# Kernel optimization log

Measured on AMD Instinct MI355X. Metric: run time of the kernel, lower is better.

Reference implementation:

```python
import jax, jax.numpy as jnp
import numpy as np

ALPHA_MIN = 1e-6
SN_EPS = 1e-6


def _spectral_normalize(W, u):
    # One power iteration (torch spectral_norm, n_power_iterations=1).
    v = W.T @ u
    v = v / (jnp.linalg.norm(v) + SN_EPS)
    u1 = W @ v
    u1 = u1 / (jnp.linalg.norm(u1) + SN_EPS)
    u1 = jax.lax.stop_gradient(u1)
    v = jax.lax.stop_gradient(v)
    sigma = u1 @ (W @ v)
    return W / sigma


def setup_inputs() -> dict:
    key = jax.random.key(0)
    ks = jax.random.split(key, 11)
    B, T, D, K = 32, 2048, 512, 128
    x = jax.random.normal(ks[0], (B, T, D), jnp.float32)
    dt = jax.random.uniform(ks[1], (B, T), jnp.float32)
    alpha_mod = jax.random.normal(ks[2], (B, T, K), jnp.float32)
    omega_mod = jax.random.normal(ks[3], (B, T, K), jnp.float32)
    tau_mod = jax.random.normal(ks[4], (B, T, 1), jnp.float32)
    s_real_raw = jax.random.normal(ks[5], (K,), jnp.float32)
    s_imag = jax.random.normal(ks[6], (K,), jnp.float32)
    tau_raw = jax.random.normal(ks[7], (1,), jnp.float32)
    W_orig = jax.random.normal(ks[8], (K, D), jnp.float32) * (1.0 / np.sqrt(D))
    b = jax.random.normal(ks[9], (K,), jnp.float32) * 0.01
    u_sn = jax.random.normal(ks[10], (K,), jnp.float32)
    u_sn = u_sn / jnp.linalg.norm(u_sn)
    return {"x": x, "dt": dt, "alpha_mod": alpha_mod, "omega_mod": omega_mod,
            "tau_mod": tau_mod, "s_real_raw": s_real_raw, "s_imag": s_imag,
            "tau_raw": tau_raw, "W_orig": W_orig, "b": b, "u_sn": u_sn}


def reference(x, dt, alpha_mod, omega_mod, tau_mod, s_real_raw, s_imag,
              tau_raw, W_orig, b, u_sn):
    B, T, D = x.shape
    K = W_orig.shape[0]

    # global timescale and poles
    tau = jax.nn.softplus(tau_raw[0]) + 1e-3
    alpha0 = (jax.nn.softplus(s_real_raw) + ALPHA_MIN) * tau  # [K]
    omega0 = s_imag * tau                                      # [K]

    # time-varying modulation (all log-scale)
    scale = jnp.exp(tau_mod)                                   # [B,T,1]
    alpha = alpha0 * jnp.exp(alpha_mod) * scale                # [B,T,K]
    omega = omega0 * jnp.exp(omega_mod) * scale                # [B,T,K]

    dt3 = dt[..., None]                                        # [B,T,1]
    rho = jnp.exp(-alpha * dt3)                                # [B,T,K]
    theta = omega * dt3
    cos_t = jnp.cos(theta)
    sin_t = jnp.sin(theta)

    # spectral-norm projection u = x @ W_sn^T + b -> [B,T,K]
    W_sn = _spectral_normalize(W_orig, u_sn)
    u = jnp.einsum('btd,kd->btk', x, W_sn) + b

    # complex recurrence: z_t = rho_t * e^{i theta_t} * z_{t-1} + u_t
    def step(carry, inp):
        c, s = carry
        rt, ct, st, ut = inp
        c_new = rt * (c * ct - s * st) + ut
        s_new = rt * (c * st + s * ct)
        return (c_new, s_new), (c_new, s_new)

    xs = (jnp.swapaxes(rho, 0, 1), jnp.swapaxes(cos_t, 0, 1),
          jnp.swapaxes(sin_t, 0, 1), jnp.swapaxes(u, 0, 1))  # [T,B,K]
    init = (jnp.zeros((B, K), u.dtype), jnp.zeros((B, K), u.dtype))
    _, (C, S) = jax.lax.scan(step, init, xs)
    C = jnp.swapaxes(C, 0, 1)  # [B,T,K]
    S = jnp.swapaxes(S, 0, 1)
    return jnp.concatenate([C, S], axis=-1)  # [B,T,2K]
```

## Files before the change

### kernel.cpp

```cpp
#include <hip/hip_runtime.h>
#include <hip/hip_bf16.h>
#include <math.h>

typedef __bf16 bf16x8 __attribute__((ext_vector_type(8)));
typedef __bf16 bf16x4 __attribute__((ext_vector_type(4)));
typedef __bf16 bf16x2 __attribute__((ext_vector_type(2)));
typedef float f32x4 __attribute__((ext_vector_type(4)));

#define B_SZ 32
#define T_SZ 2048
#define D_SZ 512
#define K_SZ 128
#define TC 32
#define NC 64

__device__ __forceinline__ float softplus_f(float x){
  return x > 20.f ? x : log1pf(expf(x));
}

__global__ __launch_bounds__(512) void sn_pi(const float* __restrict__ W,
                                             const float* __restrict__ u_sn,
                                             float* __restrict__ sig_inv){
  __shared__ float red[512];
  __shared__ float vsh[512];
  __shared__ float ush[128];
  const int t = threadIdx.x;
  if (t < 128) ush[t] = u_sn[t];
  __syncthreads();
  float t1 = 0.f;
  #pragma unroll 8
  for (int k = 0; k < K_SZ; ++k) t1 += W[k*D_SZ + t] * ush[k];
  red[t] = t1 * t1;
  __syncthreads();
  for (int s = 256; s > 0; s >>= 1){ if (t < s) red[t] += red[t+s]; __syncthreads(); }
  const float n1 = sqrtf(red[0]);
  vsh[t] = t1 / (n1 + 1e-6f);
  __syncthreads();
  float t2 = 0.f;
  if (t < 128){
    const float4* Wr = (const float4*)(W + (size_t)t * D_SZ);
    const float4* vp = (const float4*)vsh;
    #pragma unroll 8
    for (int d = 0; d < D_SZ/4; ++d){
      const float4 a = Wr[d], v = vp[d];
      t2 += a.x*v.x + a.y*v.y + a.z*v.z + a.w*v.w;
    }
  }
  __syncthreads();
  red[t] = (t < 128) ? t2*t2 : 0.f;
  __syncthreads();
  for (int s = 256; s > 0; s >>= 1){ if (t < s) red[t] += red[t+s]; __syncthreads(); }
  if (t == 0){
    const float n2sq = red[0];
    const float sigma = n2sq / (sqrtf(n2sq) + 1e-6f);
    sig_inv[0] = 1.f / sigma;
  }
}

__global__ __launch_bounds__(256) void sn_scale(const float* __restrict__ W,
                                                const float* __restrict__ sig_inv,
                                                __bf16* __restrict__ Wb){
  const float inv = sig_inv[0];
  const int i = blockIdx.x*256 + threadIdx.x;
  const float4 v = ((const float4*)W)[i];
  bf16x4 o; o[0]=(__bf16)(v.x*inv); o[1]=(__bf16)(v.y*inv);
  o[2]=(__bf16)(v.z*inv); o[3]=(__bf16)(v.w*inv);
  ((bf16x4*)Wb)[i] = o;
}

__global__ __launch_bounds__(256) void gemm_xw(const float* __restrict__ X,
                                               const __bf16* __restrict__ Wb,
                                               __bf16* __restrict__ U){
  __shared__ bf16x8 As[2][1024];
  __shared__ bf16x8 Bs[2][1024];
  const int tid = threadIdx.x;
  const int lane = tid & 63;
  const int wid = tid >> 6;
  const int wm = wid >> 1, wn = wid & 1;
  const int rowbase = blockIdx.x * 128;
  const int L15 = lane & 15, Lq = lane >> 4;
  f32x4 acc[4][4] = {};

  const int rowA = tid >> 3;
  const int cg   = tid & 7;
  const int colo = cg * 8;
  int pidx[4];
  #pragma unroll
  for (int r = 0; r < 4; ++r){
    const int row = rowA + 32*r;
    const int fb = ((row >> 4) << 1) | (cg >> 2);
    const int ll = (row & 15) | ((cg & 3) << 4);
    pidx[r] = (fb*64 + ll) ^ cg;
  }
  const float* Xb  = X  + (size_t)(rowbase + rowA)*D_SZ + colo;
  const __bf16* Bb = Wb + (size_t)rowA*D_SZ + colo;

  float4 va[4], vb[4];
  bf16x8 wreg[4];
  #pragma unroll
  for (int r = 0; r < 4; ++r){
    const float4* q = (const float4*)(Xb + (size_t)(32*r)*D_SZ);
    va[r] = q[0]; vb[r] = q[1];
    wreg[r] = *(const bf16x8*)(Bb + (size_t)(32*r)*D_SZ);
  }

  int pb = 0;
  for (int kk = 0; kk < D_SZ; kk += 64){
    #pragma unroll
    for (int r = 0; r < 4; ++r){
      bf16x8 f;
      f[0]=(__bf16)va[r].x; f[1]=(__bf16)va[r].y; f[2]=(__bf16)va[r].z; f[3]=(__bf16)va[r].w;
      f[4]=(__bf16)vb[r].x; f[5]=(__bf16)vb[r].y; f[6]=(__bf16)vb[r].z; f[7]=(__bf16)vb[r].w;
      As[pb][pidx[r]] = f;
      Bs[pb][pidx[r]] = wreg[r];
    }
    __syncthreads();
    if (kk + 64 < D_SZ){
      #pragma unroll
      for (int r = 0; r < 4; ++r){
        const float4* q = (const float4*)(Xb + (size_t)(32*r)*D_SZ + kk + 64);
        va[r] = q[0]; vb[r] = q[1];
        wreg[r] = *(const bf16x8*)(Bb + (size_t)(32*r)*D_SZ + kk + 64);
      }
    }
    #pragma unroll
    for (int s = 0; s < 2; ++s){
      bf16x8 af[4], bfr[4];
      const int swz = (s << 2) | (lane >> 4);
      #pragma unroll
      for (int ii = 0; ii < 4; ++ii){
        const int fb = ((wm*4+ii) << 1) | s;
        af[ii] = As[pb][(fb*64 + lane) ^ swz];
      }
      #pragma unroll
      for (int jj = 0; jj < 4; ++jj){
        const int fb = ((wn*4+jj) << 1) | s;
        bfr[jj] = Bs[pb][(fb*64 + lane) ^ swz];
      }
      #pragma unroll
      for (int ii = 0; ii < 4; ++ii)
        #pragma unroll
        for (int jj = 0; jj < 4; ++jj)
          acc[ii][jj] = __builtin_amdgcn_mfma_f32_16x16x32_bf16(af[ii], bfr[jj], acc[ii][jj], 0, 0, 0);
    }
    pb ^= 1;
  }
  #pragma unroll
  for (int ii = 0; ii < 4; ++ii){
    const int m = rowbase + (wm*4+ii)*16 + (Lq << 2);
    #pragma unroll
    for (int jj = 0; jj < 4; ++jj){
      const int n = (wn*4+jj)*16 + L15;
      #pragma unroll
      for (int r = 0; r < 4; ++r)
        U[(size_t)(m + r)*K_SZ + n] = (__bf16)acc[ii][jj][r];
    }
  }
}

__global__ __launch_bounds__(256) void pass_a(
    const float* __restrict__ alpha_mod, const float* __restrict__ omega_mod,
    const __bf16* __restrict__ Uarr, const float* __restrict__ dt,
    const float* __restrict__ tau_mod, const float* __restrict__ s_real,
    const float* __restrict__ s_imag, const float* __restrict__ tau_raw,
    const float* __restrict__ bvec,
    float2* __restrict__ sumA, float2* __restrict__ sumT,
    float2* __restrict__ Zr, float2* __restrict__ Zi){
  const int t = threadIdx.x;
  const int kh = t & 63;
  const int cl = t >> 6;
  const int b = blockIdx.y;
  const int c = blockIdx.x*4 + cl;
  const int t0 = c * TC;
  __shared__ float sdt[4*TC], ssc[4*TC];
  if (t < 4*TC){
    const int tg = blockIdx.x*4*TC + t;
    sdt[t] = dt[b*T_SZ + tg];
    ssc[t] = __expf(tau_mod[b*T_SZ + tg]);
  }
  __syncthreads();
  const float tau = softplus_f(tau_raw[0]) + 1e-3f;
  const float2 sr = ((const float2*)s_real)[kh];
  const float2 si = ((const float2*)s_imag)[kh];
  const float2 bk = ((const float2*)bvec)[kh];
  const float a0[2] = {(softplus_f(sr.x)+1e-6f)*tau, (softplus_f(sr.y)+1e-6f)*tau};
  const float w0[2] = {si.x*tau, si.y*tau};
  float zr[2]={0,0}, zs[2]={0,0}, sA[2]={0,0}, sT[2]={0,0};
  const float* sd = sdt + cl*TC;
  const float* ss = ssc + cl*TC;
  const size_t row = (size_t)(b*T_SZ + t0);
  const float2* amp = (const float2*)(alpha_mod + row*K_SZ) + kh;
  const float2* omp = (const float2*)(omega_mod + row*K_SZ) + kh;
  const bf16x2* up  = (const bf16x2*)(Uarr + row*K_SZ) + kh;
  #pragma unroll 4
  for (int i = 0; i < TC; ++i){
    const float2 am = amp[(size_t)i*64];
    const float2 om = omp[(size_t)i*64];
    const bf16x2 u2 = up[(size_t)i*64];
    const float scdt = ss[i] * sd[i];
    #pragma unroll
    for (int j = 0; j < 2; ++j){
      const float ad = a0[j] * __expf(j ? am.y : am.x) * scdt;
      const float th = w0[j] * __expf(j ? om.y : om.x) * scdt;
      const float rho = __expf(-ad);
      float st, ct; __sincosf(th, &st, &ct);
      const float uu = (float)u2[j] + (j ? bk.y : bk.x);
      const float nr = rho*(zr[j]*ct - zs[j]*st) + uu;
      const float ns = rho*(zr[j]*st + zs[j]*ct);
      zr[j] = nr; zs[j] = ns;
      sA[j] += ad; sT[j] += th;
    }
  }
  const size_t idx = ((size_t)(b*NC + c))*64 + kh;
  sumA[idx] = make_float2(sA[0], sA[1]);
  sumT[idx] = make_float2(sT[0], sT[1]);
  Zr[idx]   = make_float2(zr[0], zr[1]);
  Zi[idx]   = make_float2(zs[0], zs[1]);
}

__global__ __launch_bounds__(256) void pass_b(
    const float* __restrict__ sumA, const float* __restrict__ sumT,
    const float* __restrict__ Zr, const float* __restrict__ Zi,
    float* __restrict__ Cr, float* __restrict__ Ci){
  const int gwave = (blockIdx.x*256 + threadIdx.x) >> 6;
  const int lane  = threadIdx.x & 63;
  const int b  = gwave >> 7;
  const int ch = gwave & 127;
  const size_t i0 = ((size_t)(b*NC) + lane)*128 + ch;
  const float sa = sumA[i0], th = sumT[i0];
  const float r = __expf(-sa);
  float s, c; __sincosf(th, &s, &c);
  float Fr = r*c, Fi = r*s;
  float Ur = Zr[i0], Ui = Zi[i0];
  #pragma unroll
  for (int d = 1; d < 64; d <<= 1){
    const float pFr = __shfl_up(Fr, d, 64);
    const float pFi = __shfl_up(Fi, d, 64);
    const float pUr = __shfl_up(Ur, d, 64);
    const float pUi = __shfl_up(Ui, d, 64);
    if (lane >= d){
      const float nFr = Fr*pFr - Fi*pFi;
      const float nFi = Fr*pFi + Fi*pFr;
      const float nUr = Fr*pUr - Fi*pUi + Ur;
      const float nUi = Fr*pUi + Fi*pUr + Ui;
      Fr = nFr; Fi = nFi; Ur = nUr; Ui = nUi;
    }
  }
  float er = __shfl_up(Ur, 1, 64);
  float ei = __shfl_up(Ui, 1, 64);
  if (lane == 0){ er = 0.f; ei = 0.f; }
  Cr[i0] = er; Ci[i0] = ei;
}

__global__ __launch_bounds__(256) void pass_c(
    const float* __restrict__ alpha_mod, const float* __restrict__ omega_mod,
    const __bf16* __restrict__ Uarr, const float* __restrict__ dt,
    const float* __restrict__ tau_mod, const float* __restrict__ s_real,
    const float* __restrict__ s_imag, const float* __restrict__ tau_raw,
    const float* __restrict__ bvec,
    const float2* __restrict__ Cr, const float2* __restrict__ Ci,
    float* __restrict__ out){
  const int t = threadIdx.x;
  const int kh = t & 63;
  const int cl = t >> 6;
  const int b = blockIdx.y;
  const int c = blockIdx.x*4 + cl;
  const int t0 = c * TC;
  __shared__ float sdt[4*TC], ssc[4*TC];
  if (t < 4*TC){
    const int tg = blockIdx.x*4*TC + t;
    sdt[t] = dt[b*T_SZ + tg];
    ssc[t] = __expf(tau_mod[b*T_SZ + tg]);
  }
  __syncthreads();
  const float tau = softplus_f(tau_raw[0]) + 1e-3f;
  const float2 sr = ((const float2*)s_real)[kh];
  const float2 si = ((const float2*)s_imag)[kh];
  const float2 bk = ((const float2*)bvec)[kh];
  const float a0[2] = {(softplus_f(sr.x)+1e-6f)*tau, (softplus_f(sr.y)+1e-6f)*tau};
  const float w0[2] = {si.x*tau, si.y*tau};
  const size_t cidx = ((size_t)(b*NC + c))*64 + kh;
  const float2 cr = Cr[cidx], cim = Ci[cidx];
  float zr[2] = {cr.x, cr.y}, zs[2] = {cim.x, cim.y};
  const float* sd = sdt + cl*TC;
  const float* ss = ssc + cl*TC;
  const size_t row = (size_t)(b*T_SZ + t0);
  const float2* amp = (const float2*)(alpha_mod + row*K_SZ) + kh;
  const float2* omp = (const float2*)(omega_mod + row*K_SZ) + kh;
  const bf16x2* up  = (const bf16x2*)(Uarr + row*K_SZ) + kh;
  float2* outC = (float2*)(out + row*(2*K_SZ)) + kh;
  float2* outS = outC + 64;
  #pragma unroll 4
  for (int i = 0; i < TC; ++i){
    const float2 am = amp[(size_t)i*64];
    const float2 om = omp[(size_t)i*64];
    const bf16x2 u2 = up[(size_t)i*64];
    const float scdt = ss[i] * sd[i];
    #pragma unroll
    for (int j = 0; j < 2; ++j){
      const float ad = a0[j] * __expf(j ? am.y : am.x) * scdt;
      const float th = w0[j] * __expf(j ? om.y : om.x) * scdt;
      const float rho = __expf(-ad);
      float st, ct; __sincosf(th, &st, &ct);
      const float uu = (float)u2[j] + (j ? bk.y : bk.x);
      const float nr = rho*(zr[j]*ct - zs[j]*st) + uu;
      const float ns = rho*(zr[j]*st + zs[j]*ct);
      zr[j] = nr; zs[j] = ns;
    }
    outC[(size_t)i*128] = make_float2(zr[0], zr[1]);
    outS[(size_t)i*128] = make_float2(zs[0], zs[1]);
  }
}

extern "C" void kernel_launch(void* const* d_in, const int* in_sizes, int n_in,
                              void* d_out, int out_size, void* d_ws, size_t ws_size,
                              hipStream_t stream){
  (void)in_sizes; (void)n_in; (void)out_size; (void)ws_size;
  const float* x         = (const float*)d_in[0];
  const float* dt        = (const float*)d_in[1];
  const float* alpha_mod = (const float*)d_in[2];
  const float* omega_mod = (const float*)d_in[3];
  const float* tau_mod   = (const float*)d_in[4];
  const float* s_real    = (const float*)d_in[5];
  const float* s_imag    = (const float*)d_in[6];
  const float* tau_raw   = (const float*)d_in[7];
  const float* W         = (const float*)d_in[8];
  const float* bvec      = (const float*)d_in[9];
  const float* u_sn      = (const float*)d_in[10];
  float* out = (float*)d_out;

  char* w = (char*)d_ws;
  __bf16* Wb = (__bf16*)w;
  __bf16* U  = (__bf16*)(w + 131072);
  size_t off = 131072 + (size_t)B_SZ*T_SZ*K_SZ*2;
  const size_t SUMN = (size_t)B_SZ*NC*K_SZ*4;
  float2* sumA = (float2*)(w + off); off += SUMN;
  float2* sumT = (float2*)(w + off); off += SUMN;
  float2* Zr   = (float2*)(w + off); off += SUMN;
  float2* Zi   = (float2*)(w + off); off += SUMN;
  float2* Cr   = (float2*)(w + off); off += SUMN;
  float2* Ci   = (float2*)(w + off); off += SUMN;
  float* sig   = (float*)(w + off);  off += 256;

  sn_pi<<<1, 512, 0, stream>>>(W, u_sn, sig);
  sn_scale<<<64, 256, 0, stream>>>(W, sig, Wb);
  gemm_xw<<<(B_SZ*T_SZ)/128, 256, 0, stream>>>(x, Wb, U);
  pass_a<<<dim3(NC/4, B_SZ), 256, 0, stream>>>(alpha_mod, omega_mod, U, dt, tau_mod,
                                               s_real, s_imag, tau_raw, bvec,
                                               sumA, sumT, Zr, Zi);
  pass_b<<<(B_SZ*K_SZ)/4, 256, 0, stream>>>((const float*)sumA, (const float*)sumT,
                                            (const float*)Zr, (const float*)Zi,
                                            (float*)Cr, (float*)Ci);
  pass_c<<<dim3(NC/4, B_SZ), 256, 0, stream>>>(alpha_mod, omega_mod, U, dt, tau_mod,
                                               s_real, s_imag, tau_raw, bvec,
                                               Cr, Ci, out);
}
```

Baseline: 327.7 us.

## Shrink GEMM K-tile for occupancy and use one channel per thread in scan passes

The GEMM now stages 32-wide K slices instead of 64, halving shared memory and prefetch registers, and adds a min-blocks hint of 4 so more workgroups fit per CU. The swizzled LDS indexing is dropped in favour of a plain fragment layout. The chunked scan passes (pass_a, pass_c) switch from two channels per thread to one channel per thread with 128 threads per chunk, giving more parallel threads and using scalar loads and stores in place of float2. The risks are LDS bank conflicts from the removed swizzle, twice as many barriers in the GEMM, and narrower memory accesses in the scan passes.

```diff
diff --git a/kernel.cpp b/kernel.cpp
--- a/kernel.cpp
+++ b/kernel.cpp
@@ -68,11 +68,11 @@
   ((bf16x4*)Wb)[i] = o;
 }
 
-__global__ __launch_bounds__(256) void gemm_xw(const float* __restrict__ X,
-                                               const __bf16* __restrict__ Wb,
-                                               __bf16* __restrict__ U){
-  __shared__ bf16x8 As[2][1024];
-  __shared__ bf16x8 Bs[2][1024];
+__global__ __launch_bounds__(256, 4) void gemm_xw(const float* __restrict__ X,
+                                                  const __bf16* __restrict__ Wb,
+                                                  __bf16* __restrict__ U){
+  __shared__ bf16x8 As[2][512];
+  __shared__ bf16x8 Bs[2][512];
   const int tid = threadIdx.x;
   const int lane = tid & 63;
   const int wid = tid >> 6;
@@ -81,67 +81,56 @@
   const int L15 = lane & 15, Lq = lane >> 4;
   f32x4 acc[4][4] = {};
 
-  const int rowA = tid >> 3;
-  const int cg   = tid & 7;
+  const int rowA = tid >> 2;
+  const int cg   = tid & 3;
   const int colo = cg * 8;
-  int pidx[4];
+  int pidx[2];
   #pragma unroll
-  for (int r = 0; r < 4; ++r){
-    const int row = rowA + 32*r;
-    const int fb = ((row >> 4) << 1) | (cg >> 2);
-    const int ll = (row & 15) | ((cg & 3) << 4);
-    pidx[r] = (fb*64 + ll) ^ cg;
+  for (int r = 0; r < 2; ++r){
+    const int row = rowA + 64*r;
+    pidx[r] = (row >> 4)*64 + ((row & 15) | (cg << 4));
   }
   const float* Xb  = X  + (size_t)(rowbase + rowA)*D_SZ + colo;
   const __bf16* Bb = Wb + (size_t)rowA*D_SZ + colo;
 
-  float4 va[4], vb[4];
-  bf16x8 wreg[4];
+  float4 va[2][2];
+  bf16x8 wreg[2];
   #pragma unroll
-  for (int r = 0; r < 4; ++r){
-    const float4* q = (const float4*)(Xb + (size_t)(32*r)*D_SZ);
-    va[r] = q[0]; vb[r] = q[1];
-    wreg[r] = *(const bf16x8*)(Bb + (size_t)(32*r)*D_SZ);
+  for (int r = 0; r < 2; ++r){
+    const float4* q = (const float4*)(Xb + (size_t)(64*r)*D_SZ);
+    va[r][0] = q[0]; va[r][1] = q[1];
+    wreg[r] = *(const bf16x8*)(Bb + (size_t)(64*r)*D_SZ);
   }
 
   int pb = 0;
-  for (int kk = 0; kk < D_SZ; kk += 64){
+  for (int kk = 0; kk < D_SZ; kk += 32){
     #pragma unroll
-    for (int r = 0; r < 4; ++r){
+    for (int r = 0; r < 2; ++r){
       bf16x8 f;
-      f[0]=(__bf16)va[r].x; f[1]=(__bf16)va[r].y; f[2]=(__bf16)va[r].z; f[3]=(__bf16)va[r].w;
-      f[4]=(__bf16)vb[r].x; f[5]=(__bf16)vb[r].y; f[6]=(__bf16)vb[r].z; f[7]=(__bf16)vb[r].w;
+      f[0]=(__bf16)va[r][0].x; f[1]=(__bf16)va[r][0].y; f[2]=(__bf16)va[r][0].z; f[3]=(__bf16)va[r][0].w;
+      f[4]=(__bf16)va[r][1].x; f[5]=(__bf16)va[r][1].y; f[6]=(__bf16)va[r][1].z; f[7]=(__bf16)va[r][1].w;
       As[pb][pidx[r]] = f;
       Bs[pb][pidx[r]] = wreg[r];
     }
     __syncthreads();
-    if (kk + 64 < D_SZ){
+    if (kk + 32 < D_SZ){
       #pragma unroll
-      for (int r = 0; r < 4; ++r){
-        const float4* q = (const float4*)(Xb + (size_t)(32*r)*D_SZ + kk + 64);
-        va[r] = q[0]; vb[r] = q[1];
-        wreg[r] = *(const bf16x8*)(Bb + (size_t)(32*r)*D_SZ + kk + 64);
+      for (int r = 0; r < 2; ++r){
+        const float4* q = (const float4*)(Xb + (size_t)(64*r)*D_SZ + kk + 32);
+        va[r][0] = q[0]; va[r][1] = q[1];
+        wreg[r] = *(const bf16x8*)(Bb + (size_t)(64*r)*D_SZ + kk + 32);
       }
     }
+    bf16x8 af[4];
     #pragma unroll
-    for (int s = 0; s < 2; ++s){
-      bf16x8 af[4], bfr[4];
-      const int swz = (s << 2) | (lane >> 4);
-      #pragma unroll
-      for (int ii = 0; ii < 4; ++ii){
-        const int fb = ((wm*4+ii) << 1) | s;
-        af[ii] = As[pb][(fb*64 + lane) ^ swz];
-      }
-      #pragma unroll
-      for (int jj = 0; jj < 4; ++jj){
-        const int fb = ((wn*4+jj) << 1) | s;
-        bfr[jj] = Bs[pb][(fb*64 + lane) ^ swz];
-      }
+    for (int ii = 0; ii < 4; ++ii)
+      af[ii] = As[pb][(wm*4+ii)*64 + lane];
+    #pragma unroll
+    for (int jj = 0; jj < 4; ++jj){
+      const bf16x8 bv = Bs[pb][(wn*4+jj)*64 + lane];
       #pragma unroll
       for (int ii = 0; ii < 4; ++ii)
-        #pragma unroll
-        for (int jj = 0; jj < 4; ++jj)
-          acc[ii][jj] = __builtin_amdgcn_mfma_f32_16x16x32_bf16(af[ii], bfr[jj], acc[ii][jj], 0, 0, 0);
+        acc[ii][jj] = __builtin_amdgcn_mfma_f32_16x16x32_bf16(af[ii], bv, acc[ii][jj], 0, 0, 0);
     }
     pb ^= 1;
   }
@@ -164,58 +153,53 @@
     const float* __restrict__ tau_mod, const float* __restrict__ s_real,
     const float* __restrict__ s_imag, const float* __restrict__ tau_raw,
     const float* __restrict__ bvec,
-    float2* __restrict__ sumA, float2* __restrict__ sumT,
-    float2* __restrict__ Zr, float2* __restrict__ Zi){
+    float* __restrict__ sumA, float* __restrict__ sumT,
+    float* __restrict__ Zr, float* __restrict__ Zi){
   const int t = threadIdx.x;
-  const int kh = t & 63;
-  const int cl = t >> 6;
+  const int ch = t & 127;
+  const int cl = t >> 7;
   const int b = blockIdx.y;
-  const int c = blockIdx.x*4 + cl;
+  const int c = blockIdx.x*2 + cl;
   const int t0 = c * TC;
-  __shared__ float sdt[4*TC], ssc[4*TC];
-  if (t < 4*TC){
-    const int tg = blockIdx.x*4*TC + t;
+  __shared__ float sdt[2*TC], ssc[2*TC];
+  if (t < 2*TC){
+    const int tg = blockIdx.x*2*TC + t;
     sdt[t] = dt[b*T_SZ + tg];
     ssc[t] = __expf(tau_mod[b*T_SZ + tg]);
   }
   __syncthreads();
   const float tau = softplus_f(tau_raw[0]) + 1e-3f;
-  const float2 sr = ((const float2*)s_real)[kh];
-  const float2 si = ((const float2*)s_imag)[kh];
-  const float2 bk = ((const float2*)bvec)[kh];
-  const float a0[2] = {(softplus_f(sr.x)+1e-6f)*tau, (softplus_f(sr.y)+1e-6f)*tau};
-  const float w0[2] = {si.x*tau, si.y*tau};
-  float zr[2]={0,0}, zs[2]={0,0}, sA[2]={0,0}, sT[2]={0,0};
+  const float a0 = (softplus_f(s_real[ch]) + 1e-6f)*tau;
+  const float w0 = s_imag[ch]*tau;
+  const float bk = bvec[ch];
+  float zr = 0.f, zs = 0.f, sA = 0.f, sT = 0.f;
   const float* sd = sdt + cl*TC;
   const float* ss = ssc + cl*TC;
   const size_t row = (size_t)(b*T_SZ + t0);
-  const float2* amp = (const float2*)(alpha_mod + row*K_SZ) + kh;
-  const float2* omp = (const float2*)(omega_mod + row*K_SZ) + kh;
-  const bf16x2* up  = (const bf16x2*)(Uarr + row*K_SZ) + kh;
-  #pragma unroll 4
+  const float* amp = alpha_mod + row*K_SZ + ch;
+  const float* omp = omega_mod + row*K_SZ + ch;
+  const __bf16* up = Uarr + row*K_SZ + ch;
+  #pragma unroll 8
   for (int i = 0; i < TC; ++i){
-    const float2 am = amp[(size_t)i*64];
-    const float2 om = omp[(size_t)i*64];
-    const bf16x2 u2 = up[(size_t)i*64];
+    const float am = amp[(size_t)i*K_SZ];
+    const float om = omp[(size_t)i*K_SZ];
+    const float uv = (float)up[(size_t)i*K_SZ];
     const float scdt = ss[i] * sd[i];
-    #pragma unroll
-    for (int j = 0; j < 2; ++j){
-      const float ad = a0[j] * __expf(j ? am.y : am.x) * scdt;
-      const float th = w0[j] * __expf(j ? om.y : om.x) * scdt;
-      const float rho = __expf(-ad);
-      float st, ct; __sincosf(th, &st, &ct);
-      const float uu = (float)u2[j] + (j ? bk.y : bk.x);
-      const float nr = rho*(zr[j]*ct - zs[j]*st) + uu;
-      const float ns = rho*(zr[j]*st + zs[j]*ct);
-      zr[j] = nr; zs[j] = ns;
-      sA[j] += ad; sT[j] += th;
-    }
-  }
-  const size_t idx = ((size_t)(b*NC + c))*64 + kh;
-  sumA[idx] = make_float2(sA[0], sA[1]);
-  sumT[idx] = make_float2(sT[0], sT[1]);
-  Zr[idx]   = make_float2(zr[0], zr[1]);
-  Zi[idx]   = make_float2(zs[0], zs[1]);
+    const float ad = a0 * __expf(am) * scdt;
+    const float th = w0 * __expf(om) * scdt;
+    const float rho = __expf(-ad);
+    float st, ct; __sincosf(th, &st, &ct);
+    const float uu = uv + bk;
+    const float nr = rho*(zr*ct - zs*st) + uu;
+    const float ns = rho*(zr*st + zs*ct);
+    zr = nr; zs = ns;
+    sA += ad; sT += th;
+  }
+  const size_t idx = ((size_t)(b*NC + c))*K_SZ + ch;
+  sumA[idx] = sA;
+  sumT[idx] = sT;
+  Zr[idx]   = zr;
+  Zi[idx]   = zs;
 }
 
 __global__ __launch_bounds__(256) void pass_b(
@@ -258,57 +242,50 @@
     const float* __restrict__ tau_mod, const float* __restrict__ s_real,
     const float* __restrict__ s_imag, const float* __restrict__ tau_raw,
     const float* __restrict__ bvec,
-    const float2* __restrict__ Cr, const float2* __restrict__ Ci,
+    const float* __restrict__ Cr, const float* __restrict__ Ci,
     float* __restrict__ out){
   const int t = threadIdx.x;
-  const int kh = t & 63;
-  const int cl = t >> 6;
+  const int ch = t & 127;
+  const int cl = t >> 7;
   const int b = blockIdx.y;
-  const int c = blockIdx.x*4 + cl;
+  const int c = blockIdx.x*2 + cl;
   const int t0 = c * TC;
-  __shared__ float sdt[4*TC], ssc[4*TC];
-  if (t < 4*TC){
-    const int tg = blockIdx.x*4*TC + t;
+  __shared__ float sdt[2*TC], ssc[2*TC];
+  if (t < 2*TC){
+    const int tg = blockIdx.x*2*TC + t;
     sdt[t] = dt[b*T_SZ + tg];
     ssc[t] = __expf(tau_mod[b*T_SZ + tg]);
   }
   __syncthreads();
   const float tau = softplus_f(tau_raw[0]) + 1e-3f;
-  const float2 sr = ((const float2*)s_real)[kh];
-  const float2 si = ((const float2*)s_imag)[kh];
-  const float2 bk = ((const float2*)bvec)[kh];
-  const float a0[2] = {(softplus_f(sr.x)+1e-6f)*tau, (softplus_f(sr.y)+1e-6f)*tau};
-  const float w0[2] = {si.x*tau, si.y*tau};
-  const size_t cidx = ((size_t)(b*NC + c))*64 + kh;
-  const float2 cr = Cr[cidx], cim = Ci[cidx];
-  float zr[2] = {cr.x, cr.y}, zs[2] = {cim.x, cim.y};
+  const float a0 = (softplus_f(s_real[ch]) + 1e-6f)*tau;
+  const float w0 = s_imag[ch]*tau;
+  const float bk = bvec[ch];
+  const size_t cidx = ((size_t)(b*NC + c))*K_SZ + ch;
+  float zr = Cr[cidx], zs = Ci[cidx];
   const float* sd = sdt + cl*TC;
   const float* ss = ssc + cl*TC;
   const size_t row = (size_t)(b*T_SZ + t0);
-  const float2* amp = (const float2*)(alpha_mod + row*K_SZ) + kh;
-  const float2* omp = (const float2*)(omega_mod + row*K_SZ) + kh;
-  const bf16x2* up  = (const bf16x2*)(Uarr + row*K_SZ) + kh;
-  float2* outC = (float2*)(out + row*(2*K_SZ)) + kh;
-  float2* outS = outC + 64;
-  #pragma unroll 4
+  const float* amp = alpha_mod + row*K_SZ + ch;
+  const float* omp = omega_mod + row*K_SZ + ch;
+  const __bf16* up = Uarr + row*K_SZ + ch;
+  float* outp = out + row*(2*K_SZ) + ch;
+  #pragma unroll 8
   for (int i = 0; i < TC; ++i){
-    const float2 am = amp[(size_t)i*64];
-    const float2 om = omp[(size_t)i*64];
-    const bf16x2 u2 = up[(size_t)i*64];
+    const float am = amp[(size_t)i*K_SZ];
+    const float om = omp[(size_t)i*K_SZ];
+    const float uv = (float)up[(size_t)i*K_SZ];
     const float scdt = ss[i] * sd[i];
-    #pragma unroll
-    for (int j = 0; j < 2; ++j){
-      const float ad = a0[j] * __expf(j ? am.y : am.x) * scdt;
-      const float th = w0[j] * __expf(j ? om.y : om.x) * scdt;
-      const float rho = __expf(-ad);
-      float st, ct; __sincosf(th, &st, &ct);
-      const float uu = (float)u2[j] + (j ? bk.y : bk.x);
-      const float nr = rho*(zr[j]*ct - zs[j]*st) + uu;
-      const float ns = rho*(zr[j]*st + zs[j]*ct);
-      zr[j] = nr; zs[j] = ns;
-    }
-    outC[(size_t)i*128] = make_float2(zr[0], zr[1]);
-    outS[(size_t)i*128] = make_float2(zs[0], zs[1]);
+    const float ad = a0 * __expf(am) * scdt;
+    const float th = w0 * __expf(om) * scdt;
+    const float rho = __expf(-ad);
+    float st, ct; __sincosf(th, &st, &ct);
+    const float uu = uv + bk;
+    const float nr = rho*(zr*ct - zs*st) + uu;
+    const float ns = rho*(zr*st + zs*ct);
+    zr = nr; zs = ns;
+    outp[(size_t)i*(2*K_SZ)]          = zr;
+    outp[(size_t)i*(2*K_SZ) + K_SZ]   = zs;
   }
 }
 
@@ -334,24 +311,22 @@
   __bf16* U  = (__bf16*)(w + 131072);
   size_t off = 131072 + (size_t)B_SZ*T_SZ*K_SZ*2;
   const size_t SUMN = (size_t)B_SZ*NC*K_SZ*4;
-  float2* sumA = (float2*)(w + off); off += SUMN;
-  float2* sumT = (float2*)(w + off); off += SUMN;
-  float2* Zr   = (float2*)(w + off); off += SUMN;
-  float2* Zi   = (float2*)(w + off); off += SUMN;
-  float2* Cr   = (float2*)(w + off); off += SUMN;
-  float2* Ci   = (float2*)(w + off); off += SUMN;
-  float* sig   = (float*)(w + off);  off += 256;
+  float* sumA = (float*)(w + off); off += SUMN;
+  float* sumT = (float*)(w + off); off += SUMN;
+  float* Zr   = (float*)(w + off); off += SUMN;
+  float* Zi   = (float*)(w + off); off += SUMN;
+  float* Cr   = (float*)(w + off); off += SUMN;
+  float* Ci   = (float*)(w + off); off += SUMN;
+  float* sig  = (float*)(w + off); off += 256;
 
   sn_pi<<<1, 512, 0, stream>>>(W, u_sn, sig);
   sn_scale<<<64, 256, 0, stream>>>(W, sig, Wb);
   gemm_xw<<<(B_SZ*T_SZ)/128, 256, 0, stream>>>(x, Wb, U);
-  pass_a<<<dim3(NC/4, B_SZ), 256, 0, stream>>>(alpha_mod, omega_mod, U, dt, tau_mod,
+  pass_a<<<dim3(NC/2, B_SZ), 256, 0, stream>>>(alpha_mod, omega_mod, U, dt, tau_mod,
                                                s_real, s_imag, tau_raw, bvec,
                                                sumA, sumT, Zr, Zi);
-  pass_b<<<(B_SZ*K_SZ)/4, 256, 0, stream>>>((const float*)sumA, (const float*)sumT,
-                                            (const float*)Zr, (const float*)Zi,
-                                            (float*)Cr, (float*)Ci);
-  pass_c<<<dim3(NC/4, B_SZ), 256, 0, stream>>>(alpha_mod, omega_mod, U, dt, tau_mod,
+  pass_b<<<(B_SZ*K_SZ)/4, 256, 0, stream>>>(sumA, sumT, Zr, Zi, Cr, Ci);
+  pass_c<<<dim3(NC/2, B_SZ), 256, 0, stream>>>(alpha_mod, omega_mod, U, dt, tau_mod,
                                                s_real, s_imag, tau_raw, bvec,
                                                Cr, Ci, out);
 }
```

Result: slower. 341.9 us (+4.3%).

## Halve scan chunk length and have each pass_b lane combine two chunks

Applied to the files above, without the earlier changes.

Shrinks the time chunk from 32 to 16 steps, doubling the number of chunks to 128 so pass_a and pass_c launch twice as many blocks. This shortens each thread's serial recurrence. pass_b is changed so each lane first composes two adjacent chunk transforms, runs the same 64-lane wave scan, then expands the carry back to both chunks. The cost is more carry traffic and larger intermediate arrays, which adds memory work to the scan stage.

```diff
diff --git a/kernel.cpp b/kernel.cpp
--- a/kernel.cpp
+++ b/kernel.cpp
@@ -11,8 +11,8 @@
 #define T_SZ 2048
 #define D_SZ 512
 #define K_SZ 128
-#define TC 32
-#define NC 64
+#define TC 16
+#define NC 128
 
 __device__ __forceinline__ float softplus_f(float x){
   return x > 20.f ? x : log1pf(expf(x));
@@ -192,7 +192,7 @@
   const float2* amp = (const float2*)(alpha_mod + row*K_SZ) + kh;
   const float2* omp = (const float2*)(omega_mod + row*K_SZ) + kh;
   const bf16x2* up  = (const bf16x2*)(Uarr + row*K_SZ) + kh;
-  #pragma unroll 4
+  #pragma unroll 8
   for (int i = 0; i < TC; ++i){
     const float2 am = amp[(size_t)i*64];
     const float2 om = omp[(size_t)i*64];
@@ -226,12 +226,21 @@
   const int lane  = threadIdx.x & 63;
   const int b  = gwave >> 7;
   const int ch = gwave & 127;
-  const size_t i0 = ((size_t)(b*NC) + lane)*128 + ch;
-  const float sa = sumA[i0], th = sumT[i0];
-  const float r = __expf(-sa);
-  float s, c; __sincosf(th, &s, &c);
-  float Fr = r*c, Fi = r*s;
-  float Ur = Zr[i0], Ui = Zi[i0];
+  const size_t i0 = ((size_t)(b*NC) + lane*2)*128 + ch;
+  const size_t i1 = i0 + 128;
+  const float sa0 = sumA[i0], sa1 = sumA[i1];
+  const float th0 = sumT[i0], th1 = sumT[i1];
+  const float ur0 = Zr[i0],   ur1 = Zr[i1];
+  const float ui0 = Zi[i0],   ui1 = Zi[i1];
+  const float r0 = __expf(-sa0), r1 = __expf(-sa1);
+  float s0, cc0, s1, cc1;
+  __sincosf(th0, &s0, &cc0); __sincosf(th1, &s1, &cc1);
+  const float a0r = r0*cc0, a0i = r0*s0;
+  const float a1r = r1*cc1, a1i = r1*s1;
+  float Fr = a1r*a0r - a1i*a0i;
+  float Fi = a1r*a0i + a1i*a0r;
+  float Ur = a1r*ur0 - a1i*ui0 + ur1;
+  float Ui = a1r*ui0 + a1i*ur0 + ui1;
   #pragma unroll
   for (int d = 1; d < 64; d <<= 1){
     const float pFr = __shfl_up(Fr, d, 64);
@@ -246,10 +255,13 @@
       Fr = nFr; Fi = nFi; Ur = nUr; Ui = nUi;
     }
   }
-  float er = __shfl_up(Ur, 1, 64);
-  float ei = __shfl_up(Ui, 1, 64);
-  if (lane == 0){ er = 0.f; ei = 0.f; }
-  Cr[i0] = er; Ci[i0] = ei;
+  float e0r = __shfl_up(Ur, 1, 64);
+  float e0i = __shfl_up(Ui, 1, 64);
+  if (lane == 0){ e0r = 0.f; e0i = 0.f; }
+  const float e1r = a0r*e0r - a0i*e0i + ur0;
+  const float e1i = a0r*e0i + a0i*e0r + ui0;
+  Cr[i0] = e0r; Ci[i0] = e0i;
+  Cr[i1] = e1r; Ci[i1] = e1i;
 }
 
 __global__ __launch_bounds__(256) void pass_c(
@@ -290,7 +302,7 @@
   const bf16x2* up  = (const bf16x2*)(Uarr + row*K_SZ) + kh;
   float2* outC = (float2*)(out + row*(2*K_SZ)) + kh;
   float2* outS = outC + 64;
-  #pragma unroll 4
+  #pragma unroll 8
   for (int i = 0; i < TC; ++i){
     const float2 am = amp[(size_t)i*64];
     const float2 om = omp[(size_t)i*64];
```

Result: no change. 334.2 us (+2.0%).

## Fuse spectral-norm kernels and merge chunk scan into pass_a via last-block atomic

Applied to the files above, without the earlier changes.

Merges the power-iteration and weight-scaling kernels into one single-block kernel that also zeroes per-batch counters. Folds the cross-chunk prefix scan into the chunk-summary kernel: each block bumps an atomic counter for its batch, and the last block to finish runs the scan over all 128 channels. This removes two kernel launches and their gaps. In exchange, the weight scaling now runs on a single block, and the scan for each batch runs serially on one block after the others finish.

```diff
diff --git a/kernel.cpp b/kernel.cpp
--- a/kernel.cpp
+++ b/kernel.cpp
@@ -18,13 +18,15 @@
   return x > 20.f ? x : log1pf(expf(x));
 }
 
-__global__ __launch_bounds__(512) void sn_pi(const float* __restrict__ W,
-                                             const float* __restrict__ u_sn,
-                                             float* __restrict__ sig_inv){
+__global__ __launch_bounds__(512) void sn_prep(const float* __restrict__ W,
+                                               const float* __restrict__ u_sn,
+                                               __bf16* __restrict__ Wb,
+                                               unsigned* __restrict__ cnt){
   __shared__ float red[512];
   __shared__ float vsh[512];
   __shared__ float ush[128];
   const int t = threadIdx.x;
+  if (t < 32) cnt[t] = 0u;
   if (t < 128) ush[t] = u_sn[t];
   __syncthreads();
   float t1 = 0.f;
@@ -50,22 +52,15 @@
   red[t] = (t < 128) ? t2*t2 : 0.f;
   __syncthreads();
   for (int s = 256; s > 0; s >>= 1){ if (t < s) red[t] += red[t+s]; __syncthreads(); }
-  if (t == 0){
-    const float n2sq = red[0];
-    const float sigma = n2sq / (sqrtf(n2sq) + 1e-6f);
-    sig_inv[0] = 1.f / sigma;
-  }
-}
-
-__global__ __launch_bounds__(256) void sn_scale(const float* __restrict__ W,
-                                                const float* __restrict__ sig_inv,
-                                                __bf16* __restrict__ Wb){
-  const float inv = sig_inv[0];
-  const int i = blockIdx.x*256 + threadIdx.x;
-  const float4 v = ((const float4*)W)[i];
-  bf16x4 o; o[0]=(__bf16)(v.x*inv); o[1]=(__bf16)(v.y*inv);
-  o[2]=(__bf16)(v.z*inv); o[3]=(__bf16)(v.w*inv);
-  ((bf16x4*)Wb)[i] = o;
+  const float n2sq = red[0];
+  const float sigma = n2sq / (sqrtf(n2sq) + 1e-6f);
+  const float inv = 1.f / sigma;
+  for (int i = t; i < K_SZ*D_SZ/4; i += 512){
+    const float4 v = ((const float4*)W)[i];
+    bf16x4 o; o[0]=(__bf16)(v.x*inv); o[1]=(__bf16)(v.y*inv);
+    o[2]=(__bf16)(v.z*inv); o[3]=(__bf16)(v.w*inv);
+    ((bf16x4*)Wb)[i] = o;
+  }
 }
 
 __global__ __launch_bounds__(256) void gemm_xw(const float* __restrict__ X,
@@ -158,14 +153,16 @@
   }
 }
 
-__global__ __launch_bounds__(256) void pass_a(
+__global__ __launch_bounds__(256) void pass_ab(
     const float* __restrict__ alpha_mod, const float* __restrict__ omega_mod,
     const __bf16* __restrict__ Uarr, const float* __restrict__ dt,
     const float* __restrict__ tau_mod, const float* __restrict__ s_real,
     const float* __restrict__ s_imag, const float* __restrict__ tau_raw,
     const float* __restrict__ bvec,
     float2* __restrict__ sumA, float2* __restrict__ sumT,
-    float2* __restrict__ Zr, float2* __restrict__ Zi){
+    float2* __restrict__ Zr, float2* __restrict__ Zi,
+    float* __restrict__ Cr, float* __restrict__ Ci,
+    unsigned* __restrict__ cnt){
   const int t = threadIdx.x;
   const int kh = t & 63;
   const int cl = t >> 6;
@@ -216,40 +213,49 @@
   sumT[idx] = make_float2(sT[0], sT[1]);
   Zr[idx]   = make_float2(zr[0], zr[1]);
   Zi[idx]   = make_float2(zs[0], zs[1]);
-}
-
-__global__ __launch_bounds__(256) void pass_b(
-    const float* __restrict__ sumA, const float* __restrict__ sumT,
-    const float* __restrict__ Zr, const float* __restrict__ Zi,
-    float* __restrict__ Cr, float* __restrict__ Ci){
-  const int gwave = (blockIdx.x*256 + threadIdx.x) >> 6;
-  const int lane  = threadIdx.x & 63;
-  const int b  = gwave >> 7;
-  const int ch = gwave & 127;
-  const size_t i0 = ((size_t)(b*NC) + lane)*128 + ch;
-  const float sa = sumA[i0], th = sumT[i0];
-  const float r = __expf(-sa);
-  float s, c; __sincosf(th, &s, &c);
-  float Fr = r*c, Fi = r*s;
-  float Ur = Zr[i0], Ui = Zi[i0];
-  #pragma unroll
-  for (int d = 1; d < 64; d <<= 1){
-    const float pFr = __shfl_up(Fr, d, 64);
-    const float pFi = __shfl_up(Fi, d, 64);
-    const float pUr = __shfl_up(Ur, d, 64);
-    const float pUi = __shfl_up(Ui, d, 64);
-    if (lane >= d){
-      const float nFr = Fr*pFr - Fi*pFi;
-      const float nFi = Fr*pFi + Fi*pFr;
-      const float nUr = Fr*pUr - Fi*pUi + Ur;
-      const float nUi = Fr*pUi + Fi*pUr + Ui;
-      Fr = nFr; Fi = nFi; Ur = nUr; Ui = nUi;
-    }
-  }
-  float er = __shfl_up(Ur, 1, 64);
-  float ei = __shfl_up(Ui, 1, 64);
-  if (lane == 0){ er = 0.f; ei = 0.f; }
-  Cr[i0] = er; Ci[i0] = ei;
+
+  __threadfence();
+  __syncthreads();
+  __shared__ unsigned lastv;
+  if (t == 0)
+    lastv = __hip_atomic_fetch_add(&cnt[b], 1u, __ATOMIC_ACQ_REL,
+                                   __HIP_MEMORY_SCOPE_AGENT);
+  __syncthreads();
+  if (lastv != gridDim.x - 1) return;
+  __threadfence();
+
+  const float* sAf = (const float*)sumA;
+  const float* sTf = (const float*)sumT;
+  const float* zRf = (const float*)Zr;
+  const float* zIf = (const float*)Zi;
+  const int lane = t & 63;
+  const int wv = t >> 6;
+  for (int ch = wv; ch < 128; ch += 4){
+    const size_t i0 = ((size_t)(b*NC) + lane)*128 + ch;
+    const float sa = sAf[i0], th = sTf[i0];
+    const float r = __expf(-sa);
+    float s, cc; __sincosf(th, &s, &cc);
+    float Fr = r*cc, Fi = r*s;
+    float Ur = zRf[i0], Ui = zIf[i0];
+    #pragma unroll
+    for (int d = 1; d < 64; d <<= 1){
+      const float pFr = __shfl_up(Fr, d, 64);
+      const float pFi = __shfl_up(Fi, d, 64);
+      const float pUr = __shfl_up(Ur, d, 64);
+      const float pUi = __shfl_up(Ui, d, 64);
+      if (lane >= d){
+        const float nFr = Fr*pFr - Fi*pFi;
+        const float nFi = Fr*pFi + Fi*pFr;
+        const float nUr = Fr*pUr - Fi*pUi + Ur;
+        const float nUi = Fr*pUi + Fi*pUr + Ui;
+        Fr = nFr; Fi = nFi; Ur = nUr; Ui = nUi;
+      }
+    }
+    float er = __shfl_up(Ur, 1, 64);
+    float ei = __shfl_up(Ui, 1, 64);
+    if (lane == 0){ er = 0.f; ei = 0.f; }
+    Cr[i0] = er; Ci[i0] = ei;
+  }
 }
 
 __global__ __launch_bounds__(256) void pass_c(
@@ -340,17 +346,14 @@
   float2* Zi   = (float2*)(w + off); off += SUMN;
   float2* Cr   = (float2*)(w + off); off += SUMN;
   float2* Ci   = (float2*)(w + off); off += SUMN;
-  float* sig   = (float*)(w + off);  off += 256;
-
-  sn_pi<<<1, 512, 0, stream>>>(W, u_sn, sig);
-  sn_scale<<<64, 256, 0, stream>>>(W, sig, Wb);
+  unsigned* cnt = (unsigned*)(w + off); off += 256;
+
+  sn_prep<<<1, 512, 0, stream>>>(W, u_sn, Wb, cnt);
   gemm_xw<<<(B_SZ*T_SZ)/128, 256, 0, stream>>>(x, Wb, U);
-  pass_a<<<dim3(NC/4, B_SZ), 256, 0, stream>>>(alpha_mod, omega_mod, U, dt, tau_mod,
-                                               s_real, s_imag, tau_raw, bvec,
-                                               sumA, sumT, Zr, Zi);
-  pass_b<<<(B_SZ*K_SZ)/4, 256, 0, stream>>>((const float*)sumA, (const float*)sumT,
-                                            (const float*)Zr, (const float*)Zi,
-                                            (float*)Cr, (float*)Ci);
+  pass_ab<<<dim3(NC/4, B_SZ), 256, 0, stream>>>(alpha_mod, omega_mod, U, dt, tau_mod,
+                                                s_real, s_imag, tau_raw, bvec,
+                                                sumA, sumT, Zr, Zi,
+                                                (float*)Cr, (float*)Ci, cnt);
   pass_c<<<dim3(NC/4, B_SZ), 256, 0, stream>>>(alpha_mod, omega_mod, U, dt, tau_mod,
                                                s_real, s_imag, tau_raw, bvec,
                                                Cr, Ci, out);
```

Result: slower. 473.0 us (+44.3%).
